# Kernel optimization log

Measured on AMD Instinct MI355X. Metric: run time of the kernel, lower is better.

## Reference

```python
import jax, jax.numpy as jnp
from jax import lax
import numpy as np

B, S, T = 32, 512, 64
IN, H, L, HC, OUT = 512, 512, 2, 4, 512

def setup_inputs() -> dict:
    key = jax.random.key(0)
    ks = jax.random.split(key, 12)
    def w(k, shape, fan_in):
        return (jax.random.normal(k, shape, jnp.float32) / np.float32(np.sqrt(fan_in)))
    lstm_in0 = IN + HC * H
    return {
        "inputs": jax.random.normal(ks[0], (B, T, IN), jnp.float32),
        "lengths": jax.random.randint(ks[1], (B,), 1, S + 1),
        "final_hiddens": jax.random.normal(ks[2], (L, B, H), jnp.float32),
        "hiddens": jax.random.normal(ks[3], (B, S, H), jnp.float32),
        "max_output_len": T,
        "max_seq_len": S,
        "Wa1": w(ks[4], (H, 2 * H), 2 * H), "ba1": jnp.zeros((H,), jnp.float32),
        "Wa2": w(ks[5], (HC, H), H), "ba2": jnp.zeros((HC,), jnp.float32),
        "W_ih0": w(ks[6], (4 * H, lstm_in0), lstm_in0), "W_hh0": w(ks[7], (4 * H, H), H),
        "b_ih0": jnp.zeros((4 * H,), jnp.float32), "b_hh0": jnp.zeros((4 * H,), jnp.float32),
        "W_ih1": w(ks[8], (4 * H, H), H), "W_hh1": w(ks[9], (4 * H, H), H),
        "b_ih1": jnp.zeros((4 * H,), jnp.float32), "b_hh1": jnp.zeros((4 * H,), jnp.float32),
        "Wo1": w(ks[10], (H, (1 + HC) * H), (1 + HC) * H), "bo1": jnp.zeros((H,), jnp.float32),
        "Wo2": w(ks[11], (OUT, H), H), "bo2": jnp.zeros((OUT,), jnp.float32),
    }

def _lstm_cell(x, h, c, W_ih, W_hh, b_ih, b_hh):
    # PyTorch LSTM gate order: i, f, g, o
    g = x @ W_ih.T + b_ih + h @ W_hh.T + b_hh
    i, f, gg, o = jnp.split(g, 4, axis=-1)
    c_new = jax.nn.sigmoid(f) * c + jax.nn.sigmoid(i) * jnp.tanh(gg)
    h_new = jax.nn.sigmoid(o) * jnp.tanh(c_new)
    return h_new, c_new

def reference(inputs, lengths, final_hiddens, hiddens, max_output_len, max_seq_len,
              Wa1, ba1, Wa2, ba2, W_ih0, W_hh0, b_ih0, b_hh0,
              W_ih1, W_hh1, b_ih1, b_hh1, Wo1, bo1, Wo2, bo2):
    batch = inputs.shape[0]
    # r_mask[b, s] = 1 if s < lengths[b] else 0  -> [B, S, 1]
    r_mask = (jnp.arange(max_seq_len)[None, :] < lengths[:, None]).astype(hiddens.dtype)[..., None]

    def step(carry, x_t):
        h, c = carry  # each [L, B, H]
        last = h[-1]  # [B, H]
        dup = last[:, None, :] * r_mask  # [B, S, H]
        a = jax.nn.relu(jnp.concatenate([dup, hiddens], axis=2) @ Wa1.T + ba1)  # [B,S,H]
        a = jax.nn.relu(a @ Wa2.T + ba2)  # [B,S,HC]
        a = jax.nn.softmax(a, axis=1)  # softmax over seq dim (unmasked, as in source)
        c_vecs = jnp.einsum('bsk,bsh->bkh', a, hiddens).reshape(batch, -1)  # [B, HC*H]
        x = jnp.concatenate([x_t, c_vecs], axis=1)  # [B, IN + HC*H]
        h0, c0 = _lstm_cell(x, h[0], c[0], W_ih0, W_hh0, b_ih0, b_hh0)
        h1, c1 = _lstm_cell(h0, h[1], c[1], W_ih1, W_hh1, b_ih1, b_hh1)
        out = jnp.tanh(jax.nn.relu(jnp.concatenate([h1, c_vecs], axis=1) @ Wo1.T + bo1) @ Wo2.T + bo2)
        return (jnp.stack([h0, h1]), jnp.stack([c0, c1])), out

    c_init = jnp.zeros_like(final_hiddens)
    _, outs = lax.scan(step, (final_hiddens, c_init), jnp.swapaxes(inputs, 0, 1))  # [T,B,OUT]
    return jnp.swapaxes(outs, 0, 1)  # [B, T, OUT]
```

## Files before the change

### kernel.cpp

```cpp
#include <hip/hip_runtime.h>
#include <cmath>


typedef unsigned short ushort;
typedef unsigned int uint;
typedef __attribute__((ext_vector_type(8))) short bf16x8;
typedef __attribute__((ext_vector_type(4))) float f32x4;

__device__ __forceinline__ float sigmoidf_(float x) { return 1.f / (1.f + __expf(-x)); }
__device__ __forceinline__ float bf2f(ushort u) {
  union { uint i; float f; } x; x.i = ((uint)u) << 16; return x.f;
}
__device__ __forceinline__ ushort f2bf(float f) {
  union { float f; uint i; } x; x.f = f;
  return (ushort)((x.i + 0x7FFFu + ((x.i >> 16) & 1u)) >> 16);
}
__device__ __forceinline__ float wave_sum(float v) {
#pragma unroll
  for (int m = 1; m < 64; m <<= 1) v += __shfl_xor(v, m, 64);
  return v;
}
__device__ __forceinline__ float wave_max(float v) {
#pragma unroll
  for (int m = 1; m < 64; m <<= 1) v = fmaxf(v, __shfl_xor(v, m, 64));
  return v;
}

__global__ void __launch_bounds__(256) k_init(const float* __restrict__ fh,
                                              ushort* h0b0, ushort* h1b0,
                                              float* c0, float* c1) {
  int i = blockIdx.x * 256 + threadIdx.x;
  h0b0[i] = f2bf(fh[i]);
  h1b0[i] = f2bf(fh[16384 + i]);
  c0[i] = 0.f; c1[i] = 0.f;
}

__global__ void __launch_bounds__(256) k_prep(const float* __restrict__ hid,
                                              ushort* __restrict__ hbf) {
  size_t i0 = ((size_t)blockIdx.x * 256 + threadIdx.x) * 8;
  float4 f0 = *(const float4*)&hid[i0];
  float4 f1 = *(const float4*)&hid[i0 + 4];
  uint4 o;
  o.x = (uint)f2bf(f0.x) | ((uint)f2bf(f0.y) << 16);
  o.y = (uint)f2bf(f0.z) | ((uint)f2bf(f0.w) << 16);
  o.z = (uint)f2bf(f1.x) | ((uint)f2bf(f1.y) << 16);
  o.w = (uint)f2bf(f1.z) | ((uint)f2bf(f1.w) << 16);
  *(uint4*)&hbf[i0] = o;
}

__global__ void __launch_bounds__(256) k_inprep(const float* __restrict__ inputs,
                                                ushort* __restrict__ inb) {
  size_t idx4 = ((size_t)blockIdx.x * 256 + threadIdx.x) * 4;
  int m = (int)(idx4 >> 9), k = (int)(idx4 & 511);
  int b = m & 31, tt = m >> 5;
  float4 v = *(const float4*)&inputs[((size_t)b * 64 + tt) * 512 + k];
  ushort4 o; o.x = f2bf(v.x); o.y = f2bf(v.y); o.z = f2bf(v.z); o.w = f2bf(v.w);
  *(ushort4*)&inb[(size_t)m * 512 + k] = o;
}

__global__ void __launch_bounds__(256) k_wcvt(const float* __restrict__ W1, int ld1,
                                              const float* __restrict__ W2, int ld2,
                                              int split, int K,
                                              ushort* __restrict__ dst) {
  size_t idx = ((size_t)blockIdx.x * 256 + threadIdx.x) * 4;
  int j = (int)(idx / K), k = (int)(idx % K);
  const float* src = (k < split) ? (W1 + (size_t)j * ld1 + k)
                                 : (W2 + (size_t)j * ld2 + (k - split));
  float4 v = *(const float4*)src;
  ushort4 o; o.x = f2bf(v.x); o.y = f2bf(v.y); o.z = f2bf(v.z); o.w = f2bf(v.w);
  *(ushort4*)&dst[idx] = o;
}

__global__ void __launch_bounds__(256) k_hidproj(const float* __restrict__ hid,
                                                 const float* __restrict__ Wa1,
                                                 ushort* __restrict__ hpT) {
  __shared__ float As[64][33];
  __shared__ float Bs[64][33];
  int tid = threadIdx.x;
  int r0 = blockIdx.x * 64;
  int n0 = blockIdx.y * 64;
  int b = r0 >> 9, sb = r0 & 511;
  int tm = (tid >> 4) << 2, tn = (tid & 15) << 2;
  int lr = tid >> 2, lk = (tid & 3) << 3;
  float acc[4][4] = {};
  for (int k0 = 0; k0 < 512; k0 += 32) {
    float4 a0 = *(const float4*)&hid[(size_t)(r0 + lr) * 512 + k0 + lk];
    float4 a1 = *(const float4*)&hid[(size_t)(r0 + lr) * 512 + k0 + lk + 4];
    float4 b0 = *(const float4*)&Wa1[(size_t)(n0 + lr) * 1024 + 512 + k0 + lk];
    float4 b1 = *(const float4*)&Wa1[(size_t)(n0 + lr) * 1024 + 512 + k0 + lk + 4];
    __syncthreads();
    As[lr][lk+0]=a0.x; As[lr][lk+1]=a0.y; As[lr][lk+2]=a0.z; As[lr][lk+3]=a0.w;
    As[lr][lk+4]=a1.x; As[lr][lk+5]=a1.y; As[lr][lk+6]=a1.z; As[lr][lk+7]=a1.w;
    Bs[lr][lk+0]=b0.x; Bs[lr][lk+1]=b0.y; Bs[lr][lk+2]=b0.z; Bs[lr][lk+3]=b0.w;
    Bs[lr][lk+4]=b1.x; Bs[lr][lk+5]=b1.y; Bs[lr][lk+6]=b1.z; Bs[lr][lk+7]=b1.w;
    __syncthreads();
#pragma unroll 8
    for (int kk = 0; kk < 32; kk++) {
      float av[4], bv[4];
#pragma unroll
      for (int i = 0; i < 4; i++) av[i] = As[tm + i][kk];
#pragma unroll
      for (int j = 0; j < 4; j++) bv[j] = Bs[tn + j][kk];
#pragma unroll
      for (int i = 0; i < 4; i++)
#pragma unroll
        for (int j = 0; j < 4; j++) acc[i][j] += av[i] * bv[j];
    }
  }
#pragma unroll
  for (int j = 0; j < 4; j++) {
    ushort4 o;
    o.x = f2bf(acc[0][j]); o.y = f2bf(acc[1][j]);
    o.z = f2bf(acc[2][j]); o.w = f2bf(acc[3][j]);
    *(ushort4*)&hpT[((size_t)b * 512 + n0 + tn + j) * 512 + sb + tm] = o;
  }
}

__device__ __forceinline__ void scores_body(
    const ushort* __restrict__ hpT, const float* __restrict__ qb,
    const float* __restrict__ ba1, const float* __restrict__ Wa2,
    const int* __restrict__ lengths, float* __restrict__ scoresP,
    int b, int kdq, int dyn, int tid) {
  int s = tid;
  int len = dyn ? lengths[b] : 512;
  if (dyn && (tid & ~63) >= len) return;
  float m = (dyn && s < len) ? 1.f : 0.f;
  float a0 = 0.f, a1 = 0.f, a2 = 0.f, a3 = 0.f;
  int kd0 = kdq << 6;
  const ushort* hpr = hpT + ((size_t)b * 512 + kd0) * 512 + s;
#pragma unroll 4
  for (int i = 0; i < 64; i++) {
    int kd = kd0 + i;
    float hv = bf2f(hpr[(size_t)i * 512]);
    float a = fmaxf(hv + ba1[kd] + m * qb[b * 512 + kd], 0.f);
    a0 += Wa2[kd] * a;
    a1 += Wa2[512 + kd] * a;
    a2 += Wa2[1024 + kd] * a;
    a3 += Wa2[1536 + kd] * a;
  }
  float* dst = scoresP + ((size_t)(kdq * 32 + b) * 4) * 512 + s;
  dst[0] = a0; dst[512] = a1; dst[1024] = a2; dst[1536] = a3;
}

__global__ void __launch_bounds__(512) k_scst(const ushort* hpT, const float* qb,
                                              const float* ba1, const float* Wa2,
                                              const int* lengths, float* scoresP) {
  scores_body(hpT, qb, ba1, Wa2, lengths, scoresP, blockIdx.x >> 3, blockIdx.x & 7, 0,
              threadIdx.x);
}

__global__ void __launch_bounds__(512) k_sum0(const float* __restrict__ scoresP,
                                              const float* __restrict__ ba2,
                                              float* __restrict__ scores0) {
  int idx = blockIdx.x * 512 + threadIdx.x;
  int b = idx >> 11, k = (idx >> 9) & 3, s = idx & 511;
  float v = ba2[k];
#pragma unroll
  for (int q = 0; q < 8; q++) v += scoresP[((size_t)(q * 32 + b) * 4 + k) * 512 + s];
  scores0[idx] = fmaxf(v, 0.f);
}

__device__ __forceinline__ void mfma_slice(
    const ushort* __restrict__ W, int ldW, int jrow0, int jstride,
    const ushort* __restrict__ xA, int ldA, int xsplit,
    const ushort* __restrict__ xB, int ldB, int coff,
    int klo, int khi, float* __restrict__ redrow) {
  const int l = threadIdx.x & 63;
  const int r16 = l & 15, koff = (l >> 4) * 8;
  const int j = jrow0 + (r16 & 3) + (r16 >> 2) * jstride;
  const ushort* wrow = W + (size_t)j * ldW + koff;
  const ushort* a0A = xA + (size_t)r16 * ldA + koff;
  const ushort* a1A = xA + (size_t)(16 + r16) * ldA + koff;
  const ushort* a0B = xB + (size_t)r16 * ldB + koff;
  const ushort* a1B = xB + (size_t)(16 + r16) * ldB + koff;
  f32x4 acc0 = {0.f, 0.f, 0.f, 0.f}, acc1 = {0.f, 0.f, 0.f, 0.f};
#pragma unroll 4
  for (int k0 = klo; k0 < khi; k0 += 32) {
    bf16x8 av0, av1;
    if (k0 < xsplit) {
      av0 = *(const bf16x8*)(a0A + k0);
      av1 = *(const bf16x8*)(a1A + k0);
    } else {
      av0 = *(const bf16x8*)(a0B + (k0 - coff));
      av1 = *(const bf16x8*)(a1B + (k0 - coff));
    }
    bf16x8 wv = *(const bf16x8*)(wrow + k0);
    acc0 = __builtin_amdgcn_mfma_f32_16x16x32_bf16(av0, wv, acc0, 0, 0, 0);
    acc1 = __builtin_amdgcn_mfma_f32_16x16x32_bf16(av1, wv, acc1, 0, 0, 0);
  }
  const int brow = (l >> 4) << 2;
#pragma unroll
  for (int r = 0; r < 4; r++) {
    redrow[r16 * 33 + brow + r] = acc0[r];
    redrow[r16 * 33 + 16 + brow + r] = acc1[r];
  }
}

__global__ void __launch_bounds__(256) k_gin0(const ushort* __restrict__ Wg0b,
                                              const ushort* __restrict__ inb,
                                              float* __restrict__ gi0) {
  __shared__ float red[4 * 528];
  int tid = threadIdx.x, w = tid >> 6;
  int j0 = blockIdx.x * 16, m0 = blockIdx.y * 32;
  mfma_slice(Wg0b, 3072, j0, 4, inb + (size_t)m0 * 512, 512, 1 << 30,
             inb + (size_t)m0 * 512, 512, 0, w * 128, w * 128 + 128,
             red + w * 528);
  __syncthreads();
#pragma unroll
  for (int e = 0; e < 2; e++) {
    int idx = tid + e * 256;
    int j = idx >> 5, b = idx & 31;
    float v = 0.f;
#pragma unroll
    for (int ww = 0; ww < 4; ww++) v += red[ww * 528 + j * 33 + b];
    gi0[(size_t)(m0 + b) * 2048 + j0 + j] = v;
  }
}

__global__ void __launch_bounds__(512) k_qo1(
    const ushort* __restrict__ Wq, const ushort* __restrict__ Wo1,
    const ushort* __restrict__ h1cur, const ushort* __restrict__ xb,
    const float* __restrict__ bo1, float* __restrict__ qb,
    ushort* __restrict__ o1bf, int t) {
  __shared__ float red[8 * 528];
  int bid = blockIdx.x, tid = threadIdx.x, w = tid >> 6;
  if (bid < 32) {
    if (t >= 64) return;
    mfma_slice(Wq, 512, bid * 16, 4, h1cur, 512, 1 << 30, h1cur, 512, 0,
               w * 64, w * 64 + 64, red + w * 528);
    __syncthreads();
    int j = tid & 15, b = tid >> 4;
    float v = 0.f;
#pragma unroll
    for (int ww = 0; ww < 8; ww++) v += red[ww * 528 + j * 33 + b];
    qb[b * 512 + bid * 16 + j] = v;
  } else {
    if (t < 1) return;
    int jm = bid - 32;
    mfma_slice(Wo1, 2560, jm * 16, 4, h1cur, 512, 512, xb, 2048, 512,
               w * 320, w * 320 + 320, red + w * 528);
    __syncthreads();
    int j = tid & 15, b = tid >> 4;
    float v = 0.f;
#pragma unroll
    for (int ww = 0; ww < 8; ww++) v += red[ww * 528 + j * 33 + b];
    int jj = jm * 16 + j;
    o1bf[b * 512 + jj] = f2bf(fmaxf(v + bo1[jj], 0.f));
  }
}

__global__ void __launch_bounds__(512) k_scout(
    const ushort* __restrict__ hpT, const float* __restrict__ qb,
    const float* __restrict__ ba1, const float* __restrict__ Wa2,
    const int* __restrict__ lengths, float* __restrict__ scoresP,
    const ushort* __restrict__ Wo2, const ushort* __restrict__ o1bf,
    const float* __restrict__ bo2, float* __restrict__ outp, int t) {
  __shared__ float red[8 * 528];
  int bid = blockIdx.x, tid = threadIdx.x;
  if (bid < 256) {
    if (t >= 64) return;
    scores_body(hpT, qb, ba1, Wa2, lengths, scoresP, bid >> 3, bid & 7, 1, tid);
  } else {
    if (t < 1) return;
    int w = tid >> 6, jm = bid - 256;
    mfma_slice(Wo2, 512, jm * 16, 4, o1bf, 512, 1 << 30, o1bf, 512, 0,
               w * 64, w * 64 + 64, red + w * 528);
    __syncthreads();
    int j = tid & 15, b = tid >> 4;
    float v = 0.f;
#pragma unroll
    for (int ww = 0; ww < 8; ww++) v += red[ww * 528 + j * 33 + b];
    int jj = jm * 16 + j;
    outp[((size_t)b * 64 + (t - 1)) * 512 + jj] = tanhf(v + bo2[jj]);
  }
}

__global__ void __launch_bounds__(512) k_ctx(
    const float* __restrict__ scoresP, const float* __restrict__ scores0,
    const float* __restrict__ ba2, const int* __restrict__ lengths,
    const ushort* __restrict__ hbf, ushort* __restrict__ xb) {
  __shared__ float P[4 * 512];
  __shared__ float red[8 * 256];
  __shared__ float st[32], st2[32];
  int bid = blockIdx.x, tid = threadIdx.x;
  int b = bid >> 3, hs = bid & 7;
  int lane = tid & 63, w = tid >> 6;
  int s = tid, len = lengths[b];
  float v[4];
  bool act = s < len;
#pragma unroll
  for (int k = 0; k < 4; k++) {
    if (act) {
      float a = ba2[k];
#pragma unroll
      for (int q = 0; q < 8; q++)
        a += scoresP[((size_t)(q * 32 + b) * 4 + k) * 512 + s];
      v[k] = fmaxf(a, 0.f);
    } else {
      v[k] = scores0[((size_t)b * 4 + k) * 512 + s];
    }
  }
  float mx[4];
#pragma unroll
  for (int k = 0; k < 4; k++) mx[k] = wave_max(v[k]);
  if (lane == 0) {
#pragma unroll
    for (int k = 0; k < 4; k++) st[w * 4 + k] = mx[k];
  }
  __syncthreads();
#pragma unroll
  for (int k = 0; k < 4; k++) {
    float m = st[k];
#pragma unroll
    for (int w2 = 1; w2 < 8; w2++) m = fmaxf(m, st[w2 * 4 + k]);
    mx[k] = m;
  }
  float e[4];
#pragma unroll
  for (int k = 0; k < 4; k++) e[k] = __expf(v[k] - mx[k]);
  float sm[4];
#pragma unroll
  for (int k = 0; k < 4; k++) sm[k] = wave_sum(e[k]);
  if (lane == 0) {
#pragma unroll
    for (int k = 0; k < 4; k++) st2[w * 4 + k] = sm[k];
  }
  __syncthreads();
#pragma unroll
  for (int k = 0; k < 4; k++) {
    float tot = 0.f;
#pragma unroll
    for (int w2 = 0; w2 < 8; w2++) tot += st2[w2 * 4 + k];
    P[(k << 9) + s] = e[k] * (1.f / tot);
  }
  __syncthreads();
  int h = tid & 63, cch = tid >> 6;
  const ushort* hb = hbf + ((size_t)(b * 512 + (cch << 6)) * 512) + (hs << 6) + h;
  float a0 = 0.f, a1 = 0.f, a2 = 0.f, a3 = 0.f;
#pragma unroll 4
  for (int si = 0; si < 64; si++) {
    float hv = bf2f(hb[(size_t)si * 512]);
    int ps = (cch << 6) + si;
    a0 += P[ps] * hv;
    a1 += P[512 + ps] * hv;
    a2 += P[1024 + ps] * hv;
    a3 += P[1536 + ps] * hv;
  }
  red[(cch << 8) + h] = a0;
  red[(cch << 8) + 64 + h] = a1;
  red[(cch << 8) + 128 + h] = a2;
  red[(cch << 8) + 192 + h] = a3;
  __syncthreads();
  if (tid < 256) {
    int k = tid >> 6, hh = tid & 63;
    float acc = 0.f;
#pragma unroll
    for (int c = 0; c < 8; c++) acc += red[(c << 8) + (k << 6) + hh];
    xb[b * 2048 + (k << 9) + (hs << 6) + hh] = f2bf(acc);
  }
}

__global__ void __launch_bounds__(512) k_cell0(
    const ushort* __restrict__ Wg0b, const ushort* __restrict__ xb,
    const ushort* __restrict__ h0cur, const float* __restrict__ gi0,
    const float* __restrict__ bih, const float* __restrict__ bhh,
    float* __restrict__ cst, ushort* __restrict__ hnew, int t) {
  __shared__ float red[8 * 528];
  int bid = blockIdx.x, tid = threadIdx.x, w = tid >> 6;
  mfma_slice(Wg0b + 512, 3072, bid * 4, 512, xb, 2048, 2048, h0cur, 512, 2048,
             w * 320, w * 320 + 320, red + w * 528);
  __syncthreads();
  if (tid < 128) {
    int b = tid & 31, dh = tid >> 5;
    int h = bid * 4 + dh;
    float G[4];
#pragma unroll
    for (int g = 0; g < 4; g++) {
      float v = bih[g * 512 + h] + bhh[g * 512 + h] +
                gi0[(size_t)(t * 32 + b) * 2048 + g * 512 + h];
#pragma unroll
      for (int ww = 0; ww < 8; ww++) v += red[ww * 528 + (g * 4 + dh) * 33 + b];
      G[g] = v;
    }
    float i_ = sigmoidf_(G[0]), f_ = sigmoidf_(G[1]);
    float gg = tanhf(G[2]), o_ = sigmoidf_(G[3]);
    float cn = f_ * cst[b * 512 + h] + i_ * gg;
    cst[b * 512 + h] = cn;
    hnew[b * 512 + h] = f2bf(o_ * tanhf(cn));
  }
}

__global__ void __launch_bounds__(512) k_cell1(
    const ushort* __restrict__ Wg1b, const ushort* __restrict__ h0new,
    const ushort* __restrict__ h1cur, const float* __restrict__ bih,
    const float* __restrict__ bhh, float* __restrict__ cst,
    ushort* __restrict__ hnew) {
  __shared__ float red[8 * 528];
  int bid = blockIdx.x, tid = threadIdx.x, w = tid >> 6;
  mfma_slice(Wg1b, 1024, bid * 4, 512, h0new, 512, 512, h1cur, 512, 512,
             w * 128, w * 128 + 128, red + w * 528);
  __syncthreads();
  if (tid < 128) {
    int b = tid & 31, dh = tid >> 5;
    int h = bid * 4 + dh;
    float G[4];
#pragma unroll
    for (int g = 0; g < 4; g++) {
      float v = bih[g * 512 + h] + bhh[g * 512 + h];
#pragma unroll
      for (int ww = 0; ww < 8; ww++) v += red[ww * 528 + (g * 4 + dh) * 33 + b];
      G[g] = v;
    }
    float i_ = sigmoidf_(G[0]), f_ = sigmoidf_(G[1]);
    float gg = tanhf(G[2]), o_ = sigmoidf_(G[3]);
    float cn = f_ * cst[b * 512 + h] + i_ * gg;
    cst[b * 512 + h] = cn;
    hnew[b * 512 + h] = f2bf(o_ * tanhf(cn));
  }
}

extern "C" void kernel_launch(void* const* d_in, const int* in_sizes, int n_in,
                              void* d_out, int out_size, void* d_ws, size_t ws_size,
                              hipStream_t stream) {
  const float* inputs  = (const float*)d_in[0];
  const int*   lengths = (const int*)d_in[1];
  const float* fh      = (const float*)d_in[2];
  const float* hiddens = (const float*)d_in[3];
  const float* Wa1  = (const float*)d_in[6];
  const float* ba1  = (const float*)d_in[7];
  const float* Wa2  = (const float*)d_in[8];
  const float* ba2  = (const float*)d_in[9];
  const float* Wih0 = (const float*)d_in[10];
  const float* Whh0 = (const float*)d_in[11];
  const float* bih0 = (const float*)d_in[12];
  const float* bhh0 = (const float*)d_in[13];
  const float* Wih1 = (const float*)d_in[14];
  const float* Whh1 = (const float*)d_in[15];
  const float* bih1 = (const float*)d_in[16];
  const float* bhh1 = (const float*)d_in[17];
  const float* Wo1  = (const float*)d_in[18];
  const float* bo1  = (const float*)d_in[19];
  const float* Wo2  = (const float*)d_in[20];
  const float* bo2  = (const float*)d_in[21];
  float* outp = (float*)d_out;

  char* p = (char*)d_ws;
  ushort* hpT = (ushort*)p; p += (size_t)32 * 512 * 512 * 2;
  ushort* hbf = (ushort*)p; p += (size_t)32 * 512 * 512 * 2;
  float* scoresP = (float*)p; p += (size_t)8 * 32 * 4 * 512 * 4;
  float* scores0 = (float*)p; p += (size_t)32 * 4 * 512 * 4;
  float* qb      = (float*)p; p += (size_t)32 * 512 * 4;
  ushort* xb     = (ushort*)p; p += (size_t)32 * 2048 * 2;
  ushort* h0b    = (ushort*)p; p += (size_t)2 * 32 * 512 * 2;
  ushort* h1b    = (ushort*)p; p += (size_t)2 * 32 * 512 * 2;
  ushort* o1bf   = (ushort*)p; p += (size_t)32 * 512 * 2;
  float* c0      = (float*)p; p += (size_t)32 * 512 * 4;
  float* c1      = (float*)p; p += (size_t)32 * 512 * 4;
  ushort* Wg0b   = (ushort*)p; p += (size_t)2048 * 3072 * 2;
  ushort* Wg1b   = (ushort*)p; p += (size_t)2048 * 1024 * 2;
  ushort* Wo1b   = (ushort*)p; p += (size_t)512 * 2560 * 2;
  ushort* Wo2b   = (ushort*)p; p += (size_t)512 * 512 * 2;
  ushort* Wqb    = (ushort*)p; p += (size_t)512 * 512 * 2;
  ushort* inb    = (ushort*)p; p += (size_t)2048 * 512 * 2;
  float* gi0     = (float*)p; p += (size_t)2048 * 2048 * 4;

  k_init<<<64, 256, 0, stream>>>(fh, h0b, h1b, c0, c1);
  k_prep<<<4096, 256, 0, stream>>>(hiddens, hbf);
  k_inprep<<<1024, 256, 0, stream>>>(inputs, inb);
  k_hidproj<<<dim3(256, 8), 256, 0, stream>>>(hiddens, Wa1, hpT);
  k_wcvt<<<6144, 256, 0, stream>>>(Wih0, 2560, Whh0, 512, 2560, 3072, Wg0b);
  k_wcvt<<<2048, 256, 0, stream>>>(Wih1, 512, Whh1, 512, 512, 1024, Wg1b);
  k_wcvt<<<1280, 256, 0, stream>>>(Wo1, 2560, Wo1, 2560, 2560, 2560, Wo1b);
  k_wcvt<<<256, 256, 0, stream>>>(Wo2, 512, Wo2, 512, 512, 512, Wo2b);
  k_wcvt<<<256, 256, 0, stream>>>(Wa1, 1024, Wa1, 1024, 512, 512, Wqb);
  k_gin0<<<dim3(128, 64), 256, 0, stream>>>(Wg0b, inb, gi0);
  k_scst<<<256, 512, 0, stream>>>(hpT, qb, ba1, Wa2, lengths, scoresP);
  k_sum0<<<128, 512, 0, stream>>>(scoresP, ba2, scores0);

  for (int t = 0; t <= 64; t++) {
    const ushort* h1cur = h1b + (size_t)(t & 1) * 16384;
    const ushort* h0cur = h0b + (size_t)(t & 1) * 16384;
    ushort* h0nxt = h0b + (size_t)((t + 1) & 1) * 16384;
    ushort* h1nxt = h1b + (size_t)((t + 1) & 1) * 16384;
    k_qo1<<<64, 512, 0, stream>>>(Wqb, Wo1b, h1cur, xb, bo1, qb, o1bf, t);
    k_scout<<<288, 512, 0, stream>>>(hpT, qb, ba1, Wa2, lengths, scoresP,
                                     Wo2b, o1bf, bo2, outp, t);
    if (t < 64) {
      k_ctx<<<256, 512, 0, stream>>>(scoresP, scores0, ba2, lengths, hbf, xb);
      k_cell0<<<128, 512, 0, stream>>>(Wg0b, xb, h0cur, gi0, bih0, bhh0, c0,
                                       h0nxt, t);
      k_cell1<<<128, 512, 0, stream>>>(Wg1b, h0nxt, h1cur, bih1, bhh1, c1, h1nxt);
    }
  }
}
```

Baseline: 3.129 ms.

## Precompute static masked-position softmax context and fuse query projection into scores

After: 2.980 ms. -4.8%, faster.

```diff
diff --git a/kernel.cpp b/kernel.cpp
--- a/kernel.cpp
+++ b/kernel.cpp
@@ -116,23 +116,18 @@
   }
 }
 
-__device__ __forceinline__ void scores_body(
-    const ushort* __restrict__ hpT, const float* __restrict__ qb,
-    const float* __restrict__ ba1, const float* __restrict__ Wa2,
-    const int* __restrict__ lengths, float* __restrict__ scoresP,
-    int b, int kdq, int dyn, int tid) {
-  int s = tid;
-  int len = dyn ? lengths[b] : 512;
-  if (dyn && (tid & ~63) >= len) return;
-  float m = (dyn && s < len) ? 1.f : 0.f;
+__global__ void __launch_bounds__(512) k_scst(const ushort* __restrict__ hpT,
+                                              const float* __restrict__ ba1,
+                                              const float* __restrict__ Wa2,
+                                              float* __restrict__ scoresP) {
+  int bid = blockIdx.x, tid = threadIdx.x;
+  int b = bid >> 3, kdq = bid & 7, kd0 = kdq << 6, s = tid;
   float a0 = 0.f, a1 = 0.f, a2 = 0.f, a3 = 0.f;
-  int kd0 = kdq << 6;
   const ushort* hpr = hpT + ((size_t)b * 512 + kd0) * 512 + s;
 #pragma unroll 4
   for (int i = 0; i < 64; i++) {
     int kd = kd0 + i;
-    float hv = bf2f(hpr[(size_t)i * 512]);
-    float a = fmaxf(hv + ba1[kd] + m * qb[b * 512 + kd], 0.f);
+    float a = fmaxf(bf2f(hpr[(size_t)i * 512]) + ba1[kd], 0.f);
     a0 += Wa2[kd] * a;
     a1 += Wa2[512 + kd] * a;
     a2 += Wa2[1024 + kd] * a;
@@ -140,13 +135,6 @@
   }
   float* dst = scoresP + ((size_t)(kdq * 32 + b) * 4) * 512 + s;
   dst[0] = a0; dst[512] = a1; dst[1024] = a2; dst[1536] = a3;
-}
-
-__global__ void __launch_bounds__(512) k_scst(const ushort* hpT, const float* qb,
-                                              const float* ba1, const float* Wa2,
-                                              const int* lengths, float* scoresP) {
-  scores_body(hpT, qb, ba1, Wa2, lengths, scoresP, blockIdx.x >> 3, blockIdx.x & 7, 0,
-              threadIdx.x);
 }
 
 __global__ void __launch_bounds__(512) k_sum0(const float* __restrict__ scoresP,
@@ -158,6 +146,95 @@
 #pragma unroll
   for (int q = 0; q < 8; q++) v += scoresP[((size_t)(q * 32 + b) * 4 + k) * 512 + s];
   scores0[idx] = fmaxf(v, 0.f);
+}
+
+__global__ void __launch_bounds__(512) k_stat0(const float* __restrict__ scores0,
+                                               const int* __restrict__ lengths,
+                                               float* __restrict__ m0v,
+                                               float* __restrict__ statZ,
+                                               float* __restrict__ P0) {
+  __shared__ float st[32], st2[32];
+  int b = blockIdx.x, tid = threadIdx.x, lane = tid & 63, w = tid >> 6;
+  int s = tid, len = lengths[b];
+  bool stat = s >= len;
+  float v[4], m0[4];
+#pragma unroll
+  for (int k = 0; k < 4; k++) v[k] = scores0[((size_t)b * 4 + k) * 512 + s];
+#pragma unroll
+  for (int k = 0; k < 4; k++) {
+    float mk = wave_max(stat ? v[k] : -1e30f);
+    if (lane == 0) st[w * 4 + k] = mk;
+  }
+  __syncthreads();
+#pragma unroll
+  for (int k = 0; k < 4; k++) {
+    float m = st[k];
+#pragma unroll
+    for (int w2 = 1; w2 < 8; w2++) m = fmaxf(m, st[w2 * 4 + k]);
+    m0[k] = m;
+  }
+  float e[4];
+#pragma unroll
+  for (int k = 0; k < 4; k++) {
+    e[k] = stat ? __expf(v[k] - m0[k]) : 0.f;
+    float sk = wave_sum(e[k]);
+    if (lane == 0) st2[w * 4 + k] = sk;
+  }
+  __syncthreads();
+#pragma unroll
+  for (int k = 0; k < 4; k++) {
+    P0[((size_t)b * 4 + k) * 512 + s] = e[k];
+  }
+  if (tid == 0) {
+#pragma unroll
+    for (int k = 0; k < 4; k++) {
+      float z = 0.f;
+#pragma unroll
+      for (int w2 = 0; w2 < 8; w2++) z += st2[w2 * 4 + k];
+      m0v[b * 4 + k] = m0[k];
+      statZ[b * 4 + k] = z;
+    }
+  }
+}
+
+__global__ void __launch_bounds__(512) k_statvec(const float* __restrict__ P0,
+                                                 const ushort* __restrict__ hbf,
+                                                 const int* __restrict__ lengths,
+                                                 float* __restrict__ statvec) {
+  __shared__ float P[4 * 512];
+  __shared__ float red2[8 * 256];
+  int bid = blockIdx.x, tid = threadIdx.x;
+  int b = bid >> 3, hs = bid & 7;
+#pragma unroll
+  for (int k = 0; k < 4; k++) P[k * 512 + tid] = P0[((size_t)b * 4 + k) * 512 + tid];
+  __syncthreads();
+  int h = tid & 63, cch = tid >> 6;
+  int c0 = lengths[b] >> 6;
+  float a0 = 0.f, a1 = 0.f, a2 = 0.f, a3 = 0.f;
+  if (cch >= c0) {
+    const ushort* hb = hbf + ((size_t)(b * 512 + (cch << 6)) * 512) + (hs << 6) + h;
+#pragma unroll 4
+    for (int si = 0; si < 64; si++) {
+      float hv = bf2f(hb[(size_t)si * 512]);
+      int ps = (cch << 6) + si;
+      a0 += P[ps] * hv;
+      a1 += P[512 + ps] * hv;
+      a2 += P[1024 + ps] * hv;
+      a3 += P[1536 + ps] * hv;
+    }
+  }
+  red2[(cch << 8) + h] = a0;
+  red2[(cch << 8) + 64 + h] = a1;
+  red2[(cch << 8) + 128 + h] = a2;
+  red2[(cch << 8) + 192 + h] = a3;
+  __syncthreads();
+  if (tid < 256) {
+    int k = tid >> 6, hh = tid & 63;
+    float acc = 0.f;
+#pragma unroll
+    for (int c = 0; c < 8; c++) acc += red2[(c << 8) + (k << 6) + hh];
+    statvec[((size_t)b * 4 + k) * 512 + (hs << 6) + hh] = acc;
+  }
 }
 
 __device__ __forceinline__ void mfma_slice(
@@ -217,146 +294,176 @@
   }
 }
 
-__global__ void __launch_bounds__(512) k_qo1(
+__global__ void __launch_bounds__(512) k_scq(
     const ushort* __restrict__ Wq, const ushort* __restrict__ Wo1,
     const ushort* __restrict__ h1cur, const ushort* __restrict__ xb,
-    const float* __restrict__ bo1, float* __restrict__ qb,
-    ushort* __restrict__ o1bf, int t) {
+    const float* __restrict__ bo1, ushort* __restrict__ o1bf,
+    const ushort* __restrict__ hpT, const float* __restrict__ ba1,
+    const float* __restrict__ Wa2, const int* __restrict__ lengths,
+    float* __restrict__ scoresP, int t) {
   __shared__ float red[8 * 528];
-  int bid = blockIdx.x, tid = threadIdx.x, w = tid >> 6;
+  __shared__ float qs[64];
+  int bid = blockIdx.x, tid = threadIdx.x, w = tid >> 6, lane = tid & 63;
   if (bid < 32) {
-    if (t >= 64) return;
-    mfma_slice(Wq, 512, bid * 16, 4, h1cur, 512, 1 << 30, h1cur, 512, 0,
-               w * 64, w * 64 + 64, red + w * 528);
+    if (t < 1) return;
+    mfma_slice(Wo1, 2560, bid * 16, 4, h1cur, 512, 512, xb, 2048, 512,
+               w * 320, w * 320 + 320, red + w * 528);
     __syncthreads();
     int j = tid & 15, b = tid >> 4;
     float v = 0.f;
 #pragma unroll
     for (int ww = 0; ww < 8; ww++) v += red[ww * 528 + j * 33 + b];
-    qb[b * 512 + bid * 16 + j] = v;
+    int jj = bid * 16 + j;
+    o1bf[b * 512 + jj] = f2bf(fmaxf(v + bo1[jj], 0.f));
   } else {
-    if (t < 1) return;
-    int jm = bid - 32;
-    mfma_slice(Wo1, 2560, jm * 16, 4, h1cur, 512, 512, xb, 2048, 512,
-               w * 320, w * 320 + 320, red + w * 528);
-    __syncthreads();
-    int j = tid & 15, b = tid >> 4;
-    float v = 0.f;
-#pragma unroll
-    for (int ww = 0; ww < 8; ww++) v += red[ww * 528 + j * 33 + b];
-    int jj = jm * 16 + j;
-    o1bf[b * 512 + jj] = f2bf(fmaxf(v + bo1[jj], 0.f));
-  }
-}
-
-__global__ void __launch_bounds__(512) k_scout(
-    const ushort* __restrict__ hpT, const float* __restrict__ qb,
-    const float* __restrict__ ba1, const float* __restrict__ Wa2,
-    const int* __restrict__ lengths, float* __restrict__ scoresP,
+    if (t >= 64) return;
+    int r = bid - 32;
+    int b = r >> 3, kdq = r & 7, kd0 = kdq << 6;
+    {
+      bf16x8 hv8 = *(const bf16x8*)(h1cur + b * 512 + lane * 8);
+      float hf[8];
+#pragma unroll
+      for (int e2 = 0; e2 < 8; e2++) hf[e2] = bf2f(((ushort*)&hv8)[e2]);
+#pragma unroll
+      for (int rr = 0; rr < 8; rr++) {
+        int row = kd0 + w * 8 + rr;
+        bf16x8 wv8 = *(const bf16x8*)(Wq + (size_t)row * 512 + lane * 8);
+        float acc = 0.f;
+#pragma unroll
+        for (int e2 = 0; e2 < 8; e2++) acc += hf[e2] * bf2f(((ushort*)&wv8)[e2]);
+        acc = wave_sum(acc);
+        if (lane == 0) qs[w * 8 + rr] = acc;
+      }
+    }
+    __syncthreads();
+    int s = tid, len = lengths[b];
+    if ((tid & ~63) >= len) return;
+    float m = (s < len) ? 1.f : 0.f;
+    float a0 = 0.f, a1 = 0.f, a2 = 0.f, a3 = 0.f;
+    const ushort* hpr = hpT + ((size_t)b * 512 + kd0) * 512 + s;
+#pragma unroll 4
+    for (int i = 0; i < 64; i++) {
+      int kd = kd0 + i;
+      float hv = bf2f(hpr[(size_t)i * 512]);
+      float a = fmaxf(hv + ba1[kd] + m * qs[i], 0.f);
+      a0 += Wa2[kd] * a;
+      a1 += Wa2[512 + kd] * a;
+      a2 += Wa2[1024 + kd] * a;
+      a3 += Wa2[1536 + kd] * a;
+    }
+    float* dst = scoresP + ((size_t)(kdq * 32 + b) * 4) * 512 + s;
+    dst[0] = a0; dst[512] = a1; dst[1024] = a2; dst[1536] = a3;
+  }
+}
+
+__global__ void __launch_bounds__(512) k_ctxout(
+    const float* __restrict__ scoresP, const float* __restrict__ ba2,
+    const int* __restrict__ lengths, const ushort* __restrict__ hbf,
+    const float* __restrict__ m0v, const float* __restrict__ statZ,
+    const float* __restrict__ statvec, ushort* __restrict__ xb,
     const ushort* __restrict__ Wo2, const ushort* __restrict__ o1bf,
     const float* __restrict__ bo2, float* __restrict__ outp, int t) {
   __shared__ float red[8 * 528];
+  __shared__ float P[4 * 512];
+  __shared__ float red2[8 * 256];
+  __shared__ float st[32], st2[32];
   int bid = blockIdx.x, tid = threadIdx.x;
-  if (bid < 256) {
-    if (t >= 64) return;
-    scores_body(hpT, qb, ba1, Wa2, lengths, scoresP, bid >> 3, bid & 7, 1, tid);
-  } else {
+  if (bid < 32) {
     if (t < 1) return;
-    int w = tid >> 6, jm = bid - 256;
-    mfma_slice(Wo2, 512, jm * 16, 4, o1bf, 512, 1 << 30, o1bf, 512, 0,
+    int w = tid >> 6;
+    mfma_slice(Wo2, 512, bid * 16, 4, o1bf, 512, 1 << 30, o1bf, 512, 0,
                w * 64, w * 64 + 64, red + w * 528);
     __syncthreads();
     int j = tid & 15, b = tid >> 4;
     float v = 0.f;
 #pragma unroll
     for (int ww = 0; ww < 8; ww++) v += red[ww * 528 + j * 33 + b];
-    int jj = jm * 16 + j;
+    int jj = bid * 16 + j;
     outp[((size_t)b * 64 + (t - 1)) * 512 + jj] = tanhf(v + bo2[jj]);
-  }
-}
-
-__global__ void __launch_bounds__(512) k_ctx(
-    const float* __restrict__ scoresP, const float* __restrict__ scores0,
-    const float* __restrict__ ba2, const int* __restrict__ lengths,
-    const ushort* __restrict__ hbf, ushort* __restrict__ xb) {
-  __shared__ float P[4 * 512];
-  __shared__ float red[8 * 256];
-  __shared__ float st[32], st2[32];
-  int bid = blockIdx.x, tid = threadIdx.x;
-  int b = bid >> 3, hs = bid & 7;
-  int lane = tid & 63, w = tid >> 6;
-  int s = tid, len = lengths[b];
-  float v[4];
-  bool act = s < len;
-#pragma unroll
-  for (int k = 0; k < 4; k++) {
-    if (act) {
-      float a = ba2[k];
-#pragma unroll
-      for (int q = 0; q < 8; q++)
-        a += scoresP[((size_t)(q * 32 + b) * 4 + k) * 512 + s];
-      v[k] = fmaxf(a, 0.f);
-    } else {
-      v[k] = scores0[((size_t)b * 4 + k) * 512 + s];
-    }
-  }
-  float mx[4];
-#pragma unroll
-  for (int k = 0; k < 4; k++) mx[k] = wave_max(v[k]);
-  if (lane == 0) {
-#pragma unroll
-    for (int k = 0; k < 4; k++) st[w * 4 + k] = mx[k];
-  }
-  __syncthreads();
-#pragma unroll
-  for (int k = 0; k < 4; k++) {
-    float m = st[k];
-#pragma unroll
-    for (int w2 = 1; w2 < 8; w2++) m = fmaxf(m, st[w2 * 4 + k]);
-    mx[k] = m;
-  }
-  float e[4];
-#pragma unroll
-  for (int k = 0; k < 4; k++) e[k] = __expf(v[k] - mx[k]);
-  float sm[4];
-#pragma unroll
-  for (int k = 0; k < 4; k++) sm[k] = wave_sum(e[k]);
-  if (lane == 0) {
-#pragma unroll
-    for (int k = 0; k < 4; k++) st2[w * 4 + k] = sm[k];
-  }
-  __syncthreads();
-#pragma unroll
-  for (int k = 0; k < 4; k++) {
-    float tot = 0.f;
-#pragma unroll
-    for (int w2 = 0; w2 < 8; w2++) tot += st2[w2 * 4 + k];
-    P[(k << 9) + s] = e[k] * (1.f / tot);
-  }
-  __syncthreads();
-  int h = tid & 63, cch = tid >> 6;
-  const ushort* hb = hbf + ((size_t)(b * 512 + (cch << 6)) * 512) + (hs << 6) + h;
-  float a0 = 0.f, a1 = 0.f, a2 = 0.f, a3 = 0.f;
+  } else {
+    if (t >= 64) return;
+    int r = bid - 32;
+    int b = r >> 3, hs = r & 7;
+    int lane = tid & 63, w = tid >> 6;
+    int s = tid, len = lengths[b];
+    bool act = s < len;
+    float v[4];
+#pragma unroll
+    for (int k = 0; k < 4; k++) {
+      if (act) {
+        float a = ba2[k];
+#pragma unroll
+        for (int q = 0; q < 8; q++)
+          a += scoresP[((size_t)(q * 32 + b) * 4 + k) * 512 + s];
+        v[k] = fmaxf(a, 0.f);
+      } else {
+        v[k] = -1e30f;
+      }
+    }
+    float M[4];
+#pragma unroll
+    for (int k = 0; k < 4; k++) {
+      float mk = wave_max(v[k]);
+      if (lane == 0) st[w * 4 + k] = mk;
+    }
+    __syncthreads();
+#pragma unroll
+    for (int k = 0; k < 4; k++) {
+      float m = st[k];
+#pragma unroll
+      for (int w2 = 1; w2 < 8; w2++) m = fmaxf(m, st[w2 * 4 + k]);
+      M[k] = fmaxf(m, m0v[b * 4 + k]);
+    }
+    float e[4];
+#pragma unroll
+    for (int k = 0; k < 4; k++) {
+      e[k] = act ? __expf(v[k] - M[k]) : 0.f;
+      float sk = wave_sum(e[k]);
+      if (lane == 0) st2[w * 4 + k] = sk;
+    }
+    __syncthreads();
+    float sc[4];
+#pragma unroll
+    for (int k = 0; k < 4; k++) {
+      float dynZ = 0.f;
+#pragma unroll
+      for (int w2 = 0; w2 < 8; w2++) dynZ += st2[w2 * 4 + k];
+      float scB = __expf(m0v[b * 4 + k] - M[k]);
+      float Z = dynZ + scB * statZ[b * 4 + k];
+      float invZ = 1.f / Z;
+      P[(k << 9) + s] = e[k] * invZ;
+      sc[k] = scB * invZ;
+    }
+    __syncthreads();
+    int h = tid & 63, cch = tid >> 6;
+    int nch = (len + 63) >> 6;
+    float a0 = 0.f, a1 = 0.f, a2 = 0.f, a3 = 0.f;
+    if (cch < nch) {
+      const ushort* hb =
+          hbf + ((size_t)(b * 512 + (cch << 6)) * 512) + (hs << 6) + h;
 #pragma unroll 4
-  for (int si = 0; si < 64; si++) {
-    float hv = bf2f(hb[(size_t)si * 512]);
-    int ps = (cch << 6) + si;
-    a0 += P[ps] * hv;
-    a1 += P[512 + ps] * hv;
-    a2 += P[1024 + ps] * hv;
-    a3 += P[1536 + ps] * hv;
-  }
-  red[(cch << 8) + h] = a0;
-  red[(cch << 8) + 64 + h] = a1;
-  red[(cch << 8) + 128 + h] = a2;
-  red[(cch << 8) + 192 + h] = a3;
-  __syncthreads();
-  if (tid < 256) {
-    int k = tid >> 6, hh = tid & 63;
-    float acc = 0.f;
-#pragma unroll
-    for (int c = 0; c < 8; c++) acc += red[(c << 8) + (k << 6) + hh];
-    xb[b * 2048 + (k << 9) + (hs << 6) + hh] = f2bf(acc);
+      for (int si = 0; si < 64; si++) {
+        float hv = bf2f(hb[(size_t)si * 512]);
+        int ps = (cch << 6) + si;
+        a0 += P[ps] * hv;
+        a1 += P[512 + ps] * hv;
+        a2 += P[1024 + ps] * hv;
+        a3 += P[1536 + ps] * hv;
+      }
+    }
+    red2[(cch << 8) + h] = a0;
+    red2[(cch << 8) + 64 + h] = a1;
+    red2[(cch << 8) + 128 + h] = a2;
+    red2[(cch << 8) + 192 + h] = a3;
+    __syncthreads();
+    if (tid < 256) {
+      int k = tid >> 6, hh = tid & 63;
+      float acc = 0.f;
+#pragma unroll
+      for (int c = 0; c < 8; c++) acc += red2[(c << 8) + (k << 6) + hh];
+      acc += sc[k] * statvec[((size_t)b * 4 + k) * 512 + (hs << 6) + hh];
+      xb[b * 2048 + (k << 9) + (hs << 6) + hh] = f2bf(acc);
+    }
   }
 }
 
@@ -449,7 +556,10 @@
   ushort* hbf = (ushort*)p; p += (size_t)32 * 512 * 512 * 2;
   float* scoresP = (float*)p; p += (size_t)8 * 32 * 4 * 512 * 4;
   float* scores0 = (float*)p; p += (size_t)32 * 4 * 512 * 4;
-  float* qb      = (float*)p; p += (size_t)32 * 512 * 4;
+  float* P0      = (float*)p; p += (size_t)32 * 4 * 512 * 4;
+  float* statvec = (float*)p; p += (size_t)32 * 4 * 512 * 4;
+  float* m0v     = (float*)p; p += 128 * sizeof(float);
+  float* statZ   = (float*)p; p += 128 * sizeof(float);
   ushort* xb     = (ushort*)p; p += (size_t)32 * 2048 * 2;
   ushort* h0b    = (ushort*)p; p += (size_t)2 * 32 * 512 * 2;
   ushort* h1b    = (ushort*)p; p += (size_t)2 * 32 * 512 * 2;
@@ -474,19 +584,21 @@
   k_wcvt<<<256, 256, 0, stream>>>(Wo2, 512, Wo2, 512, 512, 512, Wo2b);
   k_wcvt<<<256, 256, 0, stream>>>(Wa1, 1024, Wa1, 1024, 512, 512, Wqb);
   k_gin0<<<dim3(128, 64), 256, 0, stream>>>(Wg0b, inb, gi0);
-  k_scst<<<256, 512, 0, stream>>>(hpT, qb, ba1, Wa2, lengths, scoresP);
+  k_scst<<<256, 512, 0, stream>>>(hpT, ba1, Wa2, scoresP);
   k_sum0<<<128, 512, 0, stream>>>(scoresP, ba2, scores0);
+  k_stat0<<<32, 512, 0, stream>>>(scores0, lengths, m0v, statZ, P0);
+  k_statvec<<<256, 512, 0, stream>>>(P0, hbf, lengths, statvec);
 
   for (int t = 0; t <= 64; t++) {
     const ushort* h1cur = h1b + (size_t)(t & 1) * 16384;
     const ushort* h0cur = h0b + (size_t)(t & 1) * 16384;
     ushort* h0nxt = h0b + (size_t)((t + 1) & 1) * 16384;
     ushort* h1nxt = h1b + (size_t)((t + 1) & 1) * 16384;
-    k_qo1<<<64, 512, 0, stream>>>(Wqb, Wo1b, h1cur, xb, bo1, qb, o1bf, t);
-    k_scout<<<288, 512, 0, stream>>>(hpT, qb, ba1, Wa2, lengths, scoresP,
-                                     Wo2b, o1bf, bo2, outp, t);
+    k_scq<<<288, 512, 0, stream>>>(Wqb, Wo1b, h1cur, xb, bo1, o1bf, hpT, ba1,
+                                   Wa2, lengths, scoresP, t);
+    k_ctxout<<<288, 512, 0, stream>>>(scoresP, ba2, lengths, hbf, m0v, statZ,
+                                      statvec, xb, Wo2b, o1bf, bo2, outp, t);
     if (t < 64) {
-      k_ctx<<<256, 512, 0, stream>>>(scoresP, scores0, ba2, lengths, hbf, xb);
       k_cell0<<<128, 512, 0, stream>>>(Wg0b, xb, h0cur, gi0, bih0, bhh0, c0,
                                        h0nxt, t);
       k_cell1<<<128, 512, 0, stream>>>(Wg1b, h0nxt, h1cur, bih1, bhh1, c1, h1nxt);
```
